# Performance work log

Measured on AMD Instinct MI355X. Metric: run time of the kernel, lower is better.

The kernel has to match this reference:

```python
import jax, jax.numpy as jnp
import numpy as np
from jax import lax

# Model dims (match init_kwargs): hidden=1024, H=8 heads, Dk=Dv=64, N=4 experts, top-1 read/write
H, DK, DV, N_EXP, CHUNK = 8, 64, 64, 4, 64
LORA, GATE_LR = 64, 16          # lora inner dim = head_v_dim, gate low-rank dim
NORMALIZER = 16.0               # gate_logit_normalizer
EPS = 1e-5


def chunk_gla(q, k, v, gk, C=CHUNK):
    """Chunked gated linear attention.
    q,k,gk: [L,H,Dk]; v: [L,H,Dv]; gk is per-dim log decay (<=0).
    Recurrence: S_t = diag(exp(gk_t)) S_{t-1} + k_t^T v_t ; o_t = q_t S_t.
    """
    L, h, dk = q.shape
    dv = v.shape[-1]
    nc = L // C
    qc, kc, vc, gc = (t.reshape(nc, C, h, -1) for t in (q, k, v, gk))
    g = jnp.cumsum(gc, axis=1)            # inclusive within-chunk cumsum [nc,C,h,dk]
    g_last = g[:, -1]                     # [nc,h,dk]
    qg = qc * jnp.exp(g)
    kg = kc * jnp.exp(-g)
    # intra-chunk causal part: A[t,s] = sum_d q_t,d k_s,d exp(g_t,d - g_s,d), s<=t
    A = jnp.einsum('cthd,cshd->chts', qg, kg)
    A = A * jnp.tril(jnp.ones((C, C), q.dtype))
    o_intra = jnp.einsum('chts,cshe->cthe', A, vc)
    # inter-chunk recurrence over chunk-level states
    k_out = kc * jnp.exp(g_last[:, None] - g)          # decay to chunk end
    chunk_kv = jnp.einsum('cthd,cthe->chde', k_out, vc)  # [nc,h,dk,dv]
    decay = jnp.exp(g_last)                            # [nc,h,dk]

    def step(S, inp):
        kv, dec, qg_c = inp
        o_inter = jnp.einsum('thd,hde->the', qg_c, S)
        return S * dec[..., None] + kv, o_inter

    S0 = jnp.zeros((h, dk, dv), q.dtype)
    _, o_inter = lax.scan(step, S0, (chunk_kv, decay, qg))
    return (o_intra + o_inter).reshape(L, h, dv)


def setup_inputs() -> dict:
    key = jax.random.key(0)
    ks = jax.random.split(key, 20)
    B, L, Dh = 1, 4096, 1024
    KD, VD = H * DK, H * DV
    w = lambda i, shape: jax.random.normal(ks[i], shape, jnp.float32) * 0.02
    return {
        'x': jax.random.normal(ks[0], (B, L, Dh), jnp.float32),
        'Wq': w(1, (Dh, KD)), 'Wk': w(2, (Dh, KD)), 'Wv': w(3, (Dh, VD)),
        'Wqa': w(4, (Dh, LORA)), 'Wqb': w(5, (LORA, KD)),
        'Wka': w(6, (Dh, LORA)), 'Wkb': w(7, (LORA, KD)),
        'Wg1a': w(8, (Dh, GATE_LR)), 'Wg1b': w(9, (GATE_LR, KD)), 'bg1': jnp.zeros((KD,), jnp.float32),
        'Wg2a': w(10, (Dh, GATE_LR)), 'Wg2b': w(11, (GATE_LR, KD)), 'bg2': jnp.zeros((KD,), jnp.float32),
        'We': w(12, (Dh, N_EXP)),
        'Wga': w(13, (Dh, LORA)), 'Wgb': w(14, (LORA, VD)),
        'norm_w': jnp.ones((DV,), jnp.float32),
        'Wo': w(15, (VD, Dh)),
    }


def reference(x, Wq, Wk, Wv, Wqa, Wqb, Wka, Wkb, Wg1a, Wg1b, bg1, Wg2a, Wg2b, bg2, We, Wga, Wgb, norm_w, Wo):
    B, L, Dh = x.shape
    scale = DK ** -0.5
    q1 = (x @ Wq).reshape(B, L, H, DK) * scale
    k1 = (x @ Wk).reshape(B, L, H, DK)
    v = (x @ Wv).reshape(B, L, H, DV)
    # low-rank SSE projections; use_k_softmax=True -> softmax over head dim for sparse keys
    q2 = ((x @ Wqa) @ Wqb).reshape(B, L, H, DK) * scale
    k2 = jax.nn.softmax(((x @ Wka) @ Wkb).reshape(B, L, H, DK), axis=-1)
    gk1 = (jax.nn.log_sigmoid((x @ Wg1a) @ Wg1b + bg1) / NORMALIZER).reshape(B, L, H, DK)
    gk2 = (jax.nn.log_sigmoid((x @ Wg2a) @ Wg2b + bg2) / NORMALIZER).reshape(B, L, H, DK)
    # expert routing: softmax + top-1 (num_writer=num_reader=1)
    e = jax.nn.softmax(x @ We, axis=-1)                       # [B,L,N]
    _, idx = lax.top_k(e, 1)
    mask = jax.nn.one_hot(idx, N_EXP, dtype=x.dtype).sum(-2)  # [B,L,N] write/read mask
    rw = e * mask                                             # routing prob at selected experts (emulq/emulk)
    fac = jnp.swapaxes(rw, 1, 2)[:, :, :, None, None]         # [B,N,L,1,1]
    mfac = jnp.swapaxes(mask, 1, 2)[:, :, :, None, None]
    # per-expert routed streams: tokens not routed to expert n neither write (k,gk masked) nor read (q masked)
    q_e = q2[:, None] * fac     # emulq: read gate scales q
    k_e = k2[:, None] * fac     # emulk: write gate scales k
    gk_e = gk2[:, None] * mfac  # state of expert n only decays when written
    gla_b = jax.vmap(chunk_gla)
    o_dense = gla_b(q1, k1, v, gk1)
    gla_be = jax.vmap(jax.vmap(chunk_gla, in_axes=(0, 0, None, 0)))
    o_sparse = gla_be(q_e, k_e, v, gk_e).sum(axis=1)          # sum over experts -> [B,L,H,DV]
    o = o_dense + o_sparse
    # gated RMSNorm + output projection
    g = ((x @ Wga) @ Wgb).reshape(B, L, H, DV)
    o = o * lax.rsqrt(jnp.mean(o * o, axis=-1, keepdims=True) + EPS) * norm_w
    o = o * (g * jax.nn.sigmoid(g))
    return o.reshape(B, L, H * DV) @ Wo
```

## Files before the change

### kernel.cpp

```cpp
#include <hip/hip_runtime.h>
#include <math.h>

#define LL   4096
#define HH   8
#define DK_  64
#define DV_  64
#define KD_  512
#define NEXP 4

typedef __attribute__((ext_vector_type(8))) short  s16x8;
typedef __attribute__((ext_vector_type(4))) float  f32x4;

__device__ __forceinline__ unsigned short f2bf(float f) {
    unsigned u = __float_as_uint(f);
    u += 0x7FFFu + ((u >> 16) & 1u);
    return (unsigned short)(u >> 16);
}

__device__ __forceinline__ void split2(float v, unsigned short& h, unsigned short& l) {
    h = f2bf(v);
    float hf = __uint_as_float((unsigned)h << 16);
    l = f2bf(v - hf);
}

__global__ void cvt_splitA(const float* __restrict__ in, unsigned short* __restrict__ out,
                           int n, int kshift)
{
    int i = blockIdx.x * 256 + threadIdx.x;
    if (i >= n) return;
    unsigned short h, l;
    split2(in[i], h, l);
    int K = 1 << kshift;
    int m = i >> kshift, k = i & (K - 1);
    size_t ro = (size_t)m * 3 * K;
    out[ro + k]         = h;
    out[ro + K + k]     = l;
    out[ro + 2 * K + k] = h;
}

__global__ void cvt_weights_all(
    const float* __restrict__ Wq,  const float* __restrict__ Wk,  const float* __restrict__ Wv,
    const float* __restrict__ Wqa, const float* __restrict__ Wka, const float* __restrict__ Wga,
    const float* __restrict__ Wg1a,const float* __restrict__ Wg2a,const float* __restrict__ We,
    const float* __restrict__ Wo,  const float* __restrict__ Wqb, const float* __restrict__ Wkb,
    const float* __restrict__ Wgb, const float* __restrict__ Wg1b,const float* __restrict__ Wg2b,
    unsigned short* __restrict__ WallT2, unsigned short* __restrict__ WoT2,
    unsigned short* __restrict__ WqbT2,  unsigned short* __restrict__ WkbT2,
    unsigned short* __restrict__ WgbT2,  unsigned short* __restrict__ Wg1bT2,
    unsigned short* __restrict__ Wg2bT2)
{
    int z = blockIdx.z;
    const float* W; unsigned short* WT; int K, N, ldr, pad = 0;
    switch (z) {
        case 0:  W = Wq;   WT = WallT2;                       K = 1024; N = 512;  ldr = 3072; break;
        case 1:  W = Wk;   WT = WallT2 + (size_t)512 * 3072;  K = 1024; N = 512;  ldr = 3072; break;
        case 2:  W = Wv;   WT = WallT2 + (size_t)1024 * 3072; K = 1024; N = 512;  ldr = 3072; break;
        case 3:  W = Wqa;  WT = WallT2 + (size_t)1536 * 3072; K = 1024; N = 64;   ldr = 3072; break;
        case 4:  W = Wka;  WT = WallT2 + (size_t)1600 * 3072; K = 1024; N = 64;   ldr = 3072; break;
        case 5:  W = Wga;  WT = WallT2 + (size_t)1664 * 3072; K = 1024; N = 64;   ldr = 3072; break;
        case 6:  W = Wg1a; WT = WallT2 + (size_t)1728 * 3072; K = 1024; N = 16;   ldr = 3072; break;
        case 7:  W = Wg2a; WT = WallT2 + (size_t)1744 * 3072; K = 1024; N = 16;   ldr = 3072; break;
        case 8:  W = We;   WT = WallT2 + (size_t)1760 * 3072; K = 1024; N = 4;    ldr = 3072; break;
        case 9:  W = Wo;   WT = WoT2;   K = 512; N = 1024; ldr = 1536; break;
        case 10: W = Wqb;  WT = WqbT2;  K = 64;  N = 512;  ldr = 192;  break;
        case 11: W = Wkb;  WT = WkbT2;  K = 64;  N = 512;  ldr = 192;  break;
        case 12: W = Wgb;  WT = WgbT2;  K = 64;  N = 512;  ldr = 192;  break;
        case 13: W = Wg1b; WT = Wg1bT2; K = 16;  N = 512;  ldr = 64; pad = 1; break;
        default: W = Wg2b; WT = Wg2bT2; K = 16;  N = 512;  ldr = 64; pad = 1; break;
    }
    int bx = blockIdx.x * 32, by = blockIdx.y * 32;
    if (bx >= N || by >= K) return;

    __shared__ float t[32][33];
    int x = threadIdx.x, y = threadIdx.y;
    #pragma unroll
    for (int i = 0; i < 4; ++i) {
        int kk = by + y + 8 * i;
        t[y + 8 * i][x] = (bx + x < N && kk < K) ? W[(size_t)kk * N + bx + x] : 0.f;
    }
    __syncthreads();
    #pragma unroll
    for (int i = 0; i < 4; ++i) {
        int n = bx + y + 8 * i;
        int kidx = by + x;
        if (n < N && kidx < K) {
            unsigned short h, l;
            split2(t[x][y + 8 * i], h, l);
            size_t ro = (size_t)n * ldr + kidx;
            WT[ro]         = h;
            WT[ro + K]     = h;
            WT[ro + 2 * K] = l;
        }
        if (pad && n < N && x < 16)
            WT[(size_t)n * ldr + 3 * K + x] = 0;
    }
}

__global__ __launch_bounds__(256) void gemm_qkvcat(
    const unsigned short* __restrict__ A, const unsigned short* __restrict__ B,
    float* __restrict__ Cq, float* __restrict__ Ck, float* __restrict__ Cv,
    float* __restrict__ Ct, int M, int K)
{
    __shared__ __align__(16) unsigned short sm[2 * 128 * 64];
    unsigned short* As = sm;
    unsigned short* Bs = sm + 128 * 64;

    int bxi = blockIdx.x, byi = blockIdx.y;
    {
        int gx = gridDim.x, nwg = gx * gridDim.y;
        int b = byi * gx + bxi;
        int s = (b & 7) * (nwg >> 3) + (b >> 3);
        bxi = s % gx; byi = s / gx;
    }

    int tid  = threadIdx.x;
    int lane = tid & 63;
    int w    = tid >> 6;
    int m0 = byi * 128, n0 = bxi * 128;
    int wr = w >> 1, wc = w & 1;

    f32x4 acc[4][4];
    #pragma unroll
    for (int i = 0; i < 4; ++i)
        #pragma unroll
        for (int j = 0; j < 4; ++j)
            acc[i][j] = (f32x4){0.f, 0.f, 0.f, 0.f};

    const int srow = (lane >> 3);
    const int scb  = ((lane & 7) * 16) ^ (srow << 4);

    for (int kt = 0; kt < K; kt += 64) {
        __syncthreads();
        #pragma unroll
        for (int q = 0; q < 4; ++q) {
            int r = w * 32 + q * 8 + srow;
            const char* ga = (const char*)A + ((size_t)(m0 + r) * K + kt) * 2 + scb;
            const char* gb = (const char*)B + ((size_t)(n0 + r) * K + kt) * 2 + scb;
            __builtin_amdgcn_global_load_lds(
                (const __attribute__((address_space(1))) void*)ga,
                (__attribute__((address_space(3))) void*)((char*)As + (w * 32 + q * 8) * 128),
                16, 0, 0);
            __builtin_amdgcn_global_load_lds(
                (const __attribute__((address_space(1))) void*)gb,
                (__attribute__((address_space(3))) void*)((char*)Bs + (w * 32 + q * 8) * 128),
                16, 0, 0);
        }
        __syncthreads();

        #pragma unroll
        for (int kk = 0; kk < 2; ++kk) {
            int kb = kk * 64 + (lane >> 4) * 16;
            s16x8 af[4], bfr[4];
            #pragma unroll
            for (int mi = 0; mi < 4; ++mi) {
                int r = wr * 64 + mi * 16 + (lane & 15);
                af[mi] = *(const s16x8*)((const char*)As + r * 128 + (kb ^ ((r & 7) << 4)));
            }
            #pragma unroll
            for (int ni = 0; ni < 4; ++ni) {
                int r = wc * 64 + ni * 16 + (lane & 15);
                bfr[ni] = *(const s16x8*)((const char*)Bs + r * 128 + (kb ^ ((r & 7) << 4)));
            }
            #pragma unroll
            for (int mi = 0; mi < 4; ++mi)
                #pragma unroll
                for (int ni = 0; ni < 4; ++ni)
                    acc[mi][ni] = __builtin_amdgcn_mfma_f32_16x16x32_bf16(
                        af[mi], bfr[ni], acc[mi][ni], 0, 0, 0);
        }
    }

    int base = n0 >> 9;
    float* C;
    int ldc, cb;
    if (base == 0)      { C = Cq; ldc = 512; cb = 0; }
    else if (base == 1) { C = Ck; ldc = 512; cb = 512; }
    else if (base == 2) { C = Cv; ldc = 512; cb = 1024; }
    else                { C = Ct; ldc = 256; cb = 1536; }

    #pragma unroll
    for (int mi = 0; mi < 4; ++mi)
        #pragma unroll
        for (int ni = 0; ni < 4; ++ni) {
            int col = n0 + wc * 64 + ni * 16 + (lane & 15) - cb;
            int rb  = m0 + wr * 64 + mi * 16 + (lane >> 4) * 4;
            #pragma unroll
            for (int j = 0; j < 4; ++j)
                C[(size_t)(rb + j) * ldc + col] = acc[mi][ni][j];
        }
}

__global__ __launch_bounds__(256) void gemm_mfma(
    const unsigned short* __restrict__ A0, const unsigned short* __restrict__ A1,
    const unsigned short* __restrict__ A2,
    const unsigned short* __restrict__ B0, const unsigned short* __restrict__ B1,
    const unsigned short* __restrict__ B2,
    float* __restrict__ C0, float* __restrict__ C1, float* __restrict__ C2,
    int M, int N, int K)
{
    const unsigned short* A = (blockIdx.z == 0) ? A0 : (blockIdx.z == 1) ? A1 : A2;
    const unsigned short* B = (blockIdx.z == 0) ? B0 : (blockIdx.z == 1) ? B1 : B2;
    float*                C = (blockIdx.z == 0) ? C0 : (blockIdx.z == 1) ? C1 : C2;

    __shared__ __align__(16) unsigned short sm[2 * 128 * 64];
    unsigned short* As = sm;
    unsigned short* Bs = sm + 128 * 64;

    int bxi = blockIdx.x, byi = blockIdx.y;
    {
        int gx = gridDim.x, nwg = gx * gridDim.y;
        if ((nwg & 7) == 0) {
            int b = byi * gx + bxi;
            int s = (b & 7) * (nwg >> 3) + (b >> 3);
            bxi = s % gx; byi = s / gx;
        }
    }

    int tid  = threadIdx.x;
    int lane = tid & 63;
    int w    = tid >> 6;
    int m0 = byi * 128, n0 = bxi * 128;
    int wr = w >> 1, wc = w & 1;

    f32x4 acc[4][4];
    #pragma unroll
    for (int i = 0; i < 4; ++i)
        #pragma unroll
        for (int j = 0; j < 4; ++j)
            acc[i][j] = (f32x4){0.f, 0.f, 0.f, 0.f};

    const int srow = (lane >> 3);
    const int scb  = ((lane & 7) * 16) ^ (srow << 4);

    for (int kt = 0; kt < K; kt += 64) {
        __syncthreads();
        #pragma unroll
        for (int q = 0; q < 4; ++q) {
            int r = w * 32 + q * 8 + srow;
            const char* ga = (const char*)A + ((size_t)(m0 + r) * K + kt) * 2 + scb;
            const char* gb = (const char*)B + ((size_t)(n0 + r) * K + kt) * 2 + scb;
            __builtin_amdgcn_global_load_lds(
                (const __attribute__((address_space(1))) void*)ga,
                (__attribute__((address_space(3))) void*)((char*)As + (w * 32 + q * 8) * 128),
                16, 0, 0);
            __builtin_amdgcn_global_load_lds(
                (const __attribute__((address_space(1))) void*)gb,
                (__attribute__((address_space(3))) void*)((char*)Bs + (w * 32 + q * 8) * 128),
                16, 0, 0);
        }
        __syncthreads();

        #pragma unroll
        for (int kk = 0; kk < 2; ++kk) {
            int kb = kk * 64 + (lane >> 4) * 16;
            s16x8 af[4], bfr[4];
            #pragma unroll
            for (int mi = 0; mi < 4; ++mi) {
                int r = wr * 64 + mi * 16 + (lane & 15);
                af[mi] = *(const s16x8*)((const char*)As + r * 128 + (kb ^ ((r & 7) << 4)));
            }
            #pragma unroll
            for (int ni = 0; ni < 4; ++ni) {
                int r = wc * 64 + ni * 16 + (lane & 15);
                bfr[ni] = *(const s16x8*)((const char*)Bs + r * 128 + (kb ^ ((r & 7) << 4)));
            }
            #pragma unroll
            for (int mi = 0; mi < 4; ++mi)
                #pragma unroll
                for (int ni = 0; ni < 4; ++ni)
                    acc[mi][ni] = __builtin_amdgcn_mfma_f32_16x16x32_bf16(
                        af[mi], bfr[ni], acc[mi][ni], 0, 0, 0);
        }
    }

    #pragma unroll
    for (int mi = 0; mi < 4; ++mi)
        #pragma unroll
        for (int ni = 0; ni < 4; ++ni) {
            int col = n0 + wc * 64 + ni * 16 + (lane & 15);
            int rb  = m0 + wr * 64 + mi * 16 + (lane >> 4) * 4;
            #pragma unroll
            for (int j = 0; j < 4; ++j)
                C[(size_t)(rb + j) * N + col] = acc[mi][ni][j];
        }
}

__global__ __launch_bounds__(256) void gemm_mfma5(
    const unsigned short* __restrict__ A0, const unsigned short* __restrict__ A1,
    const unsigned short* __restrict__ A2, const unsigned short* __restrict__ A3,
    const unsigned short* __restrict__ A4,
    const unsigned short* __restrict__ B0, const unsigned short* __restrict__ B1,
    const unsigned short* __restrict__ B2, const unsigned short* __restrict__ B3,
    const unsigned short* __restrict__ B4,
    float* __restrict__ C0, float* __restrict__ C1, float* __restrict__ C2,
    float* __restrict__ C3, float* __restrict__ C4, int M, int N)
{
    int z = blockIdx.z;
    const unsigned short* A = (z == 0) ? A0 : (z == 1) ? A1 : (z == 2) ? A2 : (z == 3) ? A3 : A4;
    const unsigned short* B = (z == 0) ? B0 : (z == 1) ? B1 : (z == 2) ? B2 : (z == 3) ? B3 : B4;
    float*                C = (z == 0) ? C0 : (z == 1) ? C1 : (z == 2) ? C2 : (z == 3) ? C3 : C4;
    int K = (z < 3) ? 192 : 64;

    __shared__ __align__(16) unsigned short sm[2 * 128 * 64];
    unsigned short* As = sm;
    unsigned short* Bs = sm + 128 * 64;

    int bxi = blockIdx.x, byi = blockIdx.y;
    {
        int gx = gridDim.x, nwg = gx * gridDim.y;
        if ((nwg & 7) == 0) {
            int b = byi * gx + bxi;
            int s = (b & 7) * (nwg >> 3) + (b >> 3);
            bxi = s % gx; byi = s / gx;
        }
    }

    int tid  = threadIdx.x;
    int lane = tid & 63;
    int w    = tid >> 6;
    int m0 = byi * 128, n0 = bxi * 128;
    int wr = w >> 1, wc = w & 1;

    f32x4 acc[4][4];
    #pragma unroll
    for (int i = 0; i < 4; ++i)
        #pragma unroll
        for (int j = 0; j < 4; ++j)
            acc[i][j] = (f32x4){0.f, 0.f, 0.f, 0.f};

    const int srow = (lane >> 3);
    const int scb  = ((lane & 7) * 16) ^ (srow << 4);

    for (int kt = 0; kt < K; kt += 64) {
        __syncthreads();
        #pragma unroll
        for (int q = 0; q < 4; ++q) {
            int r = w * 32 + q * 8 + srow;
            const char* ga = (const char*)A + ((size_t)(m0 + r) * K + kt) * 2 + scb;
            const char* gb = (const char*)B + ((size_t)(n0 + r) * K + kt) * 2 + scb;
            __builtin_amdgcn_global_load_lds(
                (const __attribute__((address_space(1))) void*)ga,
                (__attribute__((address_space(3))) void*)((char*)As + (w * 32 + q * 8) * 128),
                16, 0, 0);
            __builtin_amdgcn_global_load_lds(
                (const __attribute__((address_space(1))) void*)gb,
                (__attribute__((address_space(3))) void*)((char*)Bs + (w * 32 + q * 8) * 128),
                16, 0, 0);
        }
        __syncthreads();

        #pragma unroll
        for (int kk = 0; kk < 2; ++kk) {
            int kb = kk * 64 + (lane >> 4) * 16;
            s16x8 af[4], bfr[4];
            #pragma unroll
            for (int mi = 0; mi < 4; ++mi) {
                int r = wr * 64 + mi * 16 + (lane & 15);
                af[mi] = *(const s16x8*)((const char*)As + r * 128 + (kb ^ ((r & 7) << 4)));
            }
            #pragma unroll
            for (int ni = 0; ni < 4; ++ni) {
                int r = wc * 64 + ni * 16 + (lane & 15);
                bfr[ni] = *(const s16x8*)((const char*)Bs + r * 128 + (kb ^ ((r & 7) << 4)));
            }
            #pragma unroll
            for (int mi = 0; mi < 4; ++mi)
                #pragma unroll
                for (int ni = 0; ni < 4; ++ni)
                    acc[mi][ni] = __builtin_amdgcn_mfma_f32_16x16x32_bf16(
                        af[mi], bfr[ni], acc[mi][ni], 0, 0, 0);
        }
    }

    #pragma unroll
    for (int mi = 0; mi < 4; ++mi)
        #pragma unroll
        for (int ni = 0; ni < 4; ++ni) {
            int col = n0 + wc * 64 + ni * 16 + (lane & 15);
            int rb  = m0 + wr * 64 + mi * 16 + (lane >> 4) * 4;
            #pragma unroll
            for (int j = 0; j < 4; ++j)
                C[(size_t)(rb + j) * N + col] = acc[mi][ni][j];
        }
}

__global__ void unpack_cat(const float* __restrict__ tcat,
                           unsigned short* __restrict__ tqab2,
                           unsigned short* __restrict__ tkab2,
                           unsigned short* __restrict__ tgab2,
                           unsigned short* __restrict__ tg1s2,
                           unsigned short* __restrict__ tg2s2,
                           float* __restrict__ elog)
{
    int m = blockIdx.x;
    int c = threadIdx.x;
    float vx = tcat[(size_t)m * 256 + c];
    if (c < 192) {
        unsigned short h, l;
        split2(vx, h, l);
        unsigned short* dst = (c < 64) ? tqab2 : (c < 128) ? tkab2 : tgab2;
        int cc = c & 63;
        size_t ro = (size_t)m * 192;
        dst[ro + cc]       = h;
        dst[ro + 64 + cc]  = l;
        dst[ro + 128 + cc] = h;
    } else if (c < 224) {
        unsigned short h, l;
        split2(vx, h, l);
        unsigned short* dst = (c < 208) ? tg1s2 : tg2s2;
        int cc = (c - 192) & 15;
        size_t ro = (size_t)m * 64;
        dst[ro + cc]      = h;
        dst[ro + 16 + cc] = l;
        dst[ro + 32 + cc] = h;
        dst[ro + 48 + cc] = 0;
    } else if (c < 228) {
        elog[(size_t)m * 4 + (c - 224)] = vx;
    }
}

__device__ inline float logsig(float x) {
    return fminf(x, 0.f) - log1pf(expf(-fabsf(x)));
}

__global__ void elementwise_pre(float* __restrict__ q1, float* __restrict__ q2,
                                float* __restrict__ k2, float* __restrict__ gk1,
                                float* __restrict__ gk2,
                                const float* __restrict__ bg1, const float* __restrict__ bg2,
                                const float* __restrict__ elog, float* __restrict__ rw)
{
    int l = blockIdx.x;
    int tid = threadIdx.x;
    int w = tid >> 6, lane = tid & 63;
    int idx = l * KD_ + (w << 6) + lane;

    q1[idx] *= 0.125f;
    q2[idx] *= 0.125f;

    float kv = k2[idx];
    float m = kv;
    for (int s = 32; s >= 1; s >>= 1) m = fmaxf(m, __shfl_xor(m, s, 64));
    float ev = expf(kv - m);
    float ssum = ev;
    for (int s = 32; s >= 1; s >>= 1) ssum += __shfl_xor(ssum, s, 64);
    k2[idx] = ev / ssum;

    int bi = (w << 6) + lane;
    gk1[idx] = logsig(gk1[idx] + bg1[bi]) * (1.f / 16.f);
    gk2[idx] = logsig(gk2[idx] + bg2[bi]) * (1.f / 16.f);

    if (tid == 0) {
        float xs[4];
        float mm = -1e30f;
        for (int j = 0; j < 4; ++j) { xs[j] = elog[l * 4 + j]; mm = fmaxf(mm, xs[j]); }
        float s4 = 0.f;
        for (int j = 0; j < 4; ++j) { xs[j] = expf(xs[j] - mm); s4 += xs[j]; }
        for (int j = 0; j < 4; ++j) xs[j] /= s4;
        int arg = 0; float best = xs[0];
        for (int j = 1; j < 4; ++j) if (xs[j] > best) { best = xs[j]; arg = j; }
        for (int j = 0; j < 4; ++j) rw[l * 4 + j] = (j == arg) ? xs[j] : 0.f;
    }
}

__global__ void gla_kv(const float* __restrict__ k1, const float* __restrict__ k2,
                       const float* __restrict__ gk1, const float* __restrict__ gk2,
                       const float* __restrict__ v, const float* __restrict__ rw,
                       float* __restrict__ kv_all, float* __restrict__ decay_all)
{
    int flat = (blockIdx.z * 8 + blockIdx.y) * 5 + blockIdx.x;
    int sfl = (flat & 7) * 320 + (flat >> 3);
    int p = sfl % 5, h = (sfl / 5) & 7, c = sfl / 40;

    const float* kp = (p == 0) ? k1 : k2;
    const float* gp = (p == 0) ? gk1 : gk2;

    __shared__ __align__(16) unsigned short kgT[64][200];
    __shared__ __align__(16) unsigned short vT[64][200];
    __shared__ float glast[64];
    __shared__ float wrow[64];
    __shared__ float segsum[4][64];

    int tid = threadIdx.x;
    int lane = tid & 63, w = tid >> 6;
    int d = lane, seg = w;

    float gkv[16], kvv[16], vv_[16];
    #pragma unroll
    for (int i = 0; i < 16; ++i) {
        size_t base = (size_t)(c * 64 + seg * 16 + i) * KD_ + (h << 6) + d;
        gkv[i] = gp[base];
        kvv[i] = kp[base];
        vv_[i] = v[base];
    }
    if (tid < 64) {
        int lg = c * 64 + tid;
        wrow[tid] = (p == 0) ? 1.f : rw[lg * 4 + (p - 1)];
    }
    __syncthreads();

    {
        float s = 0.f;
        #pragma unroll
        for (int i = 0; i < 16; ++i) {
            int t = seg * 16 + i;
            float xg = gkv[i];
            if (p > 0 && !(wrow[t] > 0.f)) xg = 0.f;
            s += xg;
            gkv[i] = s;
        }
        segsum[seg][d] = s;
    }
    __syncthreads();
    {
        float off = 0.f, tot = 0.f;
        #pragma unroll
        for (int ss = 0; ss < 4; ++ss) {
            float x = segsum[ss][d];
            tot += x;
            if (ss < seg) off += x;
        }
        if (seg == 0) glast[d] = tot;
        #pragma unroll
        for (int i = 0; i < 16; ++i) {
            int t = seg * 16 + i;
            float g = off + gkv[i];
            float kgval = kvv[i] * wrow[t] * expf(-g);
            unsigned short hh, ll;
            split2(kgval, hh, ll);
            kgT[d][t] = hh; kgT[d][64 + t] = ll; kgT[d][128 + t] = hh;
            split2(vv_[i], hh, ll);
            vT[d][t] = hh; vT[d][64 + t] = hh; vT[d][128 + t] = ll;
        }
    }
    __syncthreads();

    size_t base = (size_t)((c * 8 + h) * 5 + p) * 4096;
    int ar = 16 * w + (lane & 15);
    int kb = (lane >> 4) * 16;
    float dec_[4];
    #pragma unroll
    for (int j = 0; j < 4; ++j) dec_[j] = expf(glast[16 * w + (lane >> 4) * 4 + j]);

    #pragma unroll
    for (int ni = 0; ni < 4; ++ni) {
        f32x4 acc = (f32x4){0.f, 0.f, 0.f, 0.f};
        int br = 16 * ni + (lane & 15);
        #pragma unroll
        for (int kk = 0; kk < 6; ++kk) {
            s16x8 af = *(const s16x8*)((const char*)&kgT[ar][0] + kk * 64 + kb);
            s16x8 bf = *(const s16x8*)((const char*)&vT[br][0] + kk * 64 + kb);
            acc = __builtin_amdgcn_mfma_f32_16x16x32_bf16(af, bf, acc, 0, 0, 0);
        }
        #pragma unroll
        for (int j = 0; j < 4; ++j) {
            int dd = 16 * w + (lane >> 4) * 4 + j;
            kv_all[base + dd * 64 + 16 * ni + (lane & 15)] = acc[j] * dec_[j];
        }
    }
    if (tid < 64) decay_all[(size_t)((c * 8 + h) * 5 + p) * 64 + tid] = expf(glast[tid]);
}

__global__ void gla_state_scan(float* __restrict__ kv, const float* __restrict__ decay)
{
    int gid = blockIdx.x * 256 + threadIdx.x;
    int sub = gid >> 6;
    const size_t stride = 8 * 5 * 64 * 64;
    float S = 0.f;
    float kvv = kv[gid];
    for (int c = 0; c < 64; ++c) {
        size_t o = (size_t)c * stride + gid;
        float nxt = (c < 63) ? kv[o + stride] : 0.f;
        float dec = decay[c * 2560 + sub];
        kv[o] = S;
        S = fmaf(dec, S, kvv);
        kvv = nxt;
    }
}

__global__ void gla_o(const float* __restrict__ q1, const float* __restrict__ q2,
                      const float* __restrict__ k1, const float* __restrict__ k2,
                      const float* __restrict__ gk1, const float* __restrict__ gk2,
                      const float* __restrict__ v, const float* __restrict__ rw,
                      const float* __restrict__ Spre,
                      float* __restrict__ o_dense, float* __restrict__ o_sparse)
{
    int flat = (blockIdx.z * 8 + blockIdx.y) * 5 + blockIdx.x;
    int sfl = (flat & 7) * 320 + (flat >> 3);
    int p = sfl % 5, h = (sfl / 5) & 7, c = sfl / 40;

    const float* qp = (p == 0) ? q1 : q2;
    const float* kp = (p == 0) ? k1 : k2;
    const float* gp = (p == 0) ? gk1 : gk2;

    __shared__ __align__(16) unsigned short qg_bf[64][72];
    __shared__ __align__(16) unsigned short kg_bf[64][72];
    __shared__ __align__(16) unsigned short A_bf[64][72];
    __shared__ __align__(16) unsigned short vT_bf[64][72];
    __shared__ __align__(16) unsigned short ST_bf[64][72];
    __shared__ float wrow[64];
    __shared__ float segsum[4][64];

    int tid = threadIdx.x;
    int lane = tid & 63, w = tid >> 6;
    int d = lane, seg = w;

    {
        float gkv[16], qv[16], kvv[16];
        #pragma unroll
        for (int i = 0; i < 16; ++i) {
            size_t base = (size_t)(c * 64 + seg * 16 + i) * KD_ + (h << 6) + d;
            gkv[i] = gp[base];
            qv[i]  = qp[base];
            kvv[i] = kp[base];
        }
        if (tid < 64) {
            int lg = c * 64 + tid;
            wrow[tid] = (p == 0) ? 1.f : rw[lg * 4 + (p - 1)];
        }
        __syncthreads();

        float s = 0.f;
        #pragma unroll
        for (int i = 0; i < 16; ++i) {
            int t = seg * 16 + i;
            float xg = gkv[i];
            if (p > 0 && !(wrow[t] > 0.f)) xg = 0.f;
            s += xg;
            gkv[i] = s;
        }
        segsum[seg][d] = s;
        __syncthreads();

        float off = 0.f;
        for (int ss = 0; ss < seg; ++ss) off += segsum[ss][d];
        #pragma unroll
        for (int i = 0; i < 16; ++i) {
            int t = seg * 16 + i;
            float g = off + gkv[i];
            float wv = wrow[t];
            qg_bf[t][d] = f2bf(qv[i] * wv * expf(g));
            kg_bf[t][d] = f2bf(kvv[i] * wv * expf(-g));
        }
    }

    {
        size_t sbase = (size_t)((c * 8 + h) * 5 + p) * 4096;
        float Sv[16], vv_[16];
        #pragma unroll
        for (int i = 0; i < 16; ++i) Sv[i] = Spre[sbase + tid + (i << 8)];
        #pragma unroll
        for (int i = 0; i < 16; ++i)
            vv_[i] = v[(size_t)(c * 64 + seg * 16 + i) * KD_ + (h << 6) + d];
        #pragma unroll
        for (int i = 0; i < 16; ++i) ST_bf[d][4 * i + seg] = f2bf(Sv[i]);
        #pragma unroll
        for (int i = 0; i < 16; ++i) vT_bf[d][seg * 16 + i] = f2bf(vv_[i]);
    }
    __syncthreads();

    int am = 16 * w + (lane & 15);
    int kb = (lane >> 4) * 16;

    #pragma unroll
    for (int ni = 0; ni < 4; ++ni) {
        f32x4 acc = (f32x4){0.f, 0.f, 0.f, 0.f};
        if (ni <= w) {
            int br = 16 * ni + (lane & 15);
            #pragma unroll
            for (int kk = 0; kk < 2; ++kk) {
                s16x8 af = *(const s16x8*)((const char*)&qg_bf[am][0] + kk * 64 + kb);
                s16x8 bf = *(const s16x8*)((const char*)&kg_bf[br][0] + kk * 64 + kb);
                acc = __builtin_amdgcn_mfma_f32_16x16x32_bf16(af, bf, acc, 0, 0, 0);
            }
        }
        #pragma unroll
        for (int j = 0; j < 4; ++j) {
            int t = 16 * w + (lane >> 4) * 4 + j;
            int s = 16 * ni + (lane & 15);
            A_bf[t][s] = (s <= t) ? f2bf(acc[j]) : (unsigned short)0;
        }
    }
    __syncthreads();

    #pragma unroll
    for (int ni = 0; ni < 4; ++ni) {
        f32x4 acc = (f32x4){0.f, 0.f, 0.f, 0.f};
        int br = 16 * ni + (lane & 15);
        #pragma unroll
        for (int kk = 0; kk < 2; ++kk) {
            s16x8 af = *(const s16x8*)((const char*)&qg_bf[am][0] + kk * 64 + kb);
            s16x8 bf = *(const s16x8*)((const char*)&ST_bf[br][0] + kk * 64 + kb);
            acc = __builtin_amdgcn_mfma_f32_16x16x32_bf16(af, bf, acc, 0, 0, 0);
        }
        #pragma unroll
        for (int kk = 0; kk < 2; ++kk) {
            s16x8 af = *(const s16x8*)((const char*)&A_bf[am][0] + kk * 64 + kb);
            s16x8 bf = *(const s16x8*)((const char*)&vT_bf[br][0] + kk * 64 + kb);
            acc = __builtin_amdgcn_mfma_f32_16x16x32_bf16(af, bf, acc, 0, 0, 0);
        }
        #pragma unroll
        for (int j = 0; j < 4; ++j) {
            int t = 16 * w + (lane >> 4) * 4 + j;
            int e = 16 * ni + (lane & 15);
            size_t idx = (size_t)(c * 64 + t) * KD_ + (h << 6) + e;
            if (p == 0)                 o_dense[idx]  = acc[j];
            else if (wrow[t] > 0.f)     o_sparse[idx] = acc[j];
        }
    }
}

__global__ void postnorm(const float* __restrict__ o_dense, const float* __restrict__ o_sparse,
                         const float* __restrict__ gbuf,
                         const float* __restrict__ norm_w, unsigned short* __restrict__ og2)
{
    int l = blockIdx.x;
    int tid = threadIdx.x;
    int w = tid >> 6, lane = tid & 63;
    int bi = (w << 6) + lane;
    int idx = l * KD_ + bi;
    float o = o_dense[idx] + o_sparse[idx];
    float ss = o * o;
    for (int s = 32; s >= 1; s >>= 1) ss += __shfl_xor(ss, s, 64);
    float r = rsqrtf(ss * (1.f / 64.f) + 1e-5f);
    float val = o * r * norm_w[lane];
    float gv = gbuf[idx];
    val *= gv / (1.f + expf(-gv));
    unsigned short h, lo;
    split2(val, h, lo);
    size_t ro = (size_t)l * (3 * KD_) + bi;
    og2[ro]           = h;
    og2[ro + KD_]     = lo;
    og2[ro + 2 * KD_] = h;
}

extern "C" void kernel_launch(void* const* d_in, const int* in_sizes, int n_in,
                              void* d_out, int out_size, void* d_ws, size_t ws_size,
                              hipStream_t stream)
{
    const float* x    = (const float*)d_in[0];
    const float* Wq   = (const float*)d_in[1];
    const float* Wk   = (const float*)d_in[2];
    const float* Wv   = (const float*)d_in[3];
    const float* Wqa  = (const float*)d_in[4];
    const float* Wqb  = (const float*)d_in[5];
    const float* Wka  = (const float*)d_in[6];
    const float* Wkb  = (const float*)d_in[7];
    const float* Wg1a = (const float*)d_in[8];
    const float* Wg1b = (const float*)d_in[9];
    const float* bg1  = (const float*)d_in[10];
    const float* Wg2a = (const float*)d_in[11];
    const float* Wg2b = (const float*)d_in[12];
    const float* bg2  = (const float*)d_in[13];
    const float* We   = (const float*)d_in[14];
    const float* Wga  = (const float*)d_in[15];
    const float* Wgb  = (const float*)d_in[16];
    const float* normw= (const float*)d_in[17];
    const float* Wo   = (const float*)d_in[18];

    float* ws = (float*)d_ws;
    const size_t LKD = (size_t)LL * KD_;
    float* q1   = ws;
    float* k1   = q1 + LKD;
    float* v    = k1 + LKD;
    float* q2   = v  + LKD;
    float* k2   = q2 + LKD;
    float* gk1  = k2 + LKD;
    float* gk2  = gk1 + LKD;
    float* o_dense  = gk2 + LKD;
    float* o_sparse = o_dense + LKD;
    float* gbuf = o_sparse + LKD;
    float* elog = gbuf + LKD;
    float* rw   = elog + (size_t)LL * 4;
    float* kv_all    = rw + (size_t)LL * 4;
    float* decay_all = kv_all + (size_t)64 * 8 * 5 * 64 * 64;

    unsigned short* bp = (unsigned short*)(decay_all + 163840);
    unsigned short* WallT2 = bp; bp += (size_t)1792 * 3072;
    unsigned short* WoT2   = bp; bp += (size_t)1024 * 1536;
    unsigned short* WqbT2  = bp; bp += (size_t)512 * 192;
    unsigned short* WkbT2  = bp; bp += (size_t)512 * 192;
    unsigned short* WgbT2  = bp; bp += (size_t)512 * 192;
    unsigned short* Wg1bT2 = bp; bp += (size_t)512 * 64;
    unsigned short* Wg2bT2 = bp; bp += (size_t)512 * 64;
    unsigned short* tqab2  = bp; bp += (size_t)LL * 192;
    unsigned short* tkab2  = bp; bp += (size_t)LL * 192;
    unsigned short* tgab2  = bp; bp += (size_t)LL * 192;
    unsigned short* tg1s2  = bp; bp += (size_t)LL * 64;
    unsigned short* tg2s2  = bp; bp += (size_t)LL * 64;
    float* tcat = (float*)bp;

    unsigned short* xb2 = (unsigned short*)kv_all;
    unsigned short* og2 = (unsigned short*)kv_all;

    dim3 blk(256);
    dim3 tblk(32, 8);

    cvt_splitA<<<dim3((LL * 1024 + 255) / 256), blk, 0, stream>>>(x, xb2, LL * 1024, 10);
    hipMemsetAsync(WallT2 + (size_t)1764 * 3072, 0, (size_t)(1792 - 1764) * 3072 * 2, stream);
    cvt_weights_all<<<dim3(32, 32, 15), tblk, 0, stream>>>(
        Wq, Wk, Wv, Wqa, Wka, Wga, Wg1a, Wg2a, We, Wo, Wqb, Wkb, Wgb, Wg1b, Wg2b,
        WallT2, WoT2, WqbT2, WkbT2, WgbT2, Wg1bT2, Wg2bT2);

    gemm_qkvcat<<<dim3(14, 32), blk, 0, stream>>>(xb2, WallT2, q1, k1, v, tcat, LL, 3072);
    unpack_cat<<<dim3(LL), blk, 0, stream>>>(tcat, tqab2, tkab2, tgab2, tg1s2, tg2s2, elog);

    gemm_mfma5<<<dim3(4, 32, 5), blk, 0, stream>>>(
        tqab2, tkab2, tgab2, tg1s2, tg2s2,
        WqbT2, WkbT2, WgbT2, Wg1bT2, Wg2bT2,
        q2, k2, gbuf, gk1, gk2, LL, KD_);

    elementwise_pre<<<LL, 512, 0, stream>>>(q1, q2, k2, gk1, gk2, bg1, bg2, elog, rw);

    gla_kv<<<dim3(5, 8, 64), blk, 0, stream>>>(k1, k2, gk1, gk2, v, rw, kv_all, decay_all);
    gla_state_scan<<<dim3(640), blk, 0, stream>>>(kv_all, decay_all);
    gla_o<<<dim3(5, 8, 64), blk, 0, stream>>>(q1, q2, k1, k2, gk1, gk2, v, rw,
                                              kv_all, o_dense, o_sparse);

    postnorm<<<LL, 512, 0, stream>>>(o_dense, o_sparse, gbuf, normw, og2);

    gemm_mfma<<<dim3(8, 32, 1), blk, 0, stream>>>(og2, og2, og2, WoT2, WoT2, WoT2,
                                                  (float*)d_out, (float*)d_out, (float*)d_out,
                                                  LL, 1024, 1536);
}
```

Measured before the change: 231.7 us.

## Double-buffer GEMM LDS tiles and fuse elementwise prep into GEMM epilogues

All three MFMA GEMM kernels now use two LDS buffers, prefetching the next K tile with global_load_lds while MFMAs run on the current one, so each iteration needs one barrier instead of two. The q scaling, the gate bias add with logsigmoid and the normalizer are moved into the GEMM epilogues. The leftover elementwise kernel becomes a smaller softmax and router kernel, which saves a read-modify-write pass over q1, q2, gk1 and gk2. In exchange, LDS per block doubles to 64KB, which may lower occupancy.

```diff
diff --git a/kernel.cpp b/kernel.cpp
--- a/kernel.cpp
+++ b/kernel.cpp
@@ -21,6 +21,10 @@
     h = f2bf(v);
     float hf = __uint_as_float((unsigned)h << 16);
     l = f2bf(v - hf);
+}
+
+__device__ __forceinline__ float logsig(float x) {
+    return fminf(x, 0.f) - log1pf(expf(-fabsf(x)));
 }
 
 __global__ void cvt_splitA(const float* __restrict__ in, unsigned short* __restrict__ out,
@@ -101,9 +105,7 @@
     float* __restrict__ Cq, float* __restrict__ Ck, float* __restrict__ Cv,
     float* __restrict__ Ct, int M, int K)
 {
-    __shared__ __align__(16) unsigned short sm[2 * 128 * 64];
-    unsigned short* As = sm;
-    unsigned short* Bs = sm + 128 * 64;
+    __shared__ __align__(16) unsigned short sm[4 * 128 * 64];
 
     int bxi = blockIdx.x, byi = blockIdx.y;
     {
@@ -129,8 +131,9 @@
     const int srow = (lane >> 3);
     const int scb  = ((lane & 7) * 16) ^ (srow << 4);
 
-    for (int kt = 0; kt < K; kt += 64) {
-        __syncthreads();
+    auto stage = [&](int buf, int kt) {
+        unsigned short* Asb = sm + buf * (2 * 128 * 64);
+        unsigned short* Bsb = Asb + 128 * 64;
         #pragma unroll
         for (int q = 0; q < 4; ++q) {
             int r = w * 32 + q * 8 + srow;
@@ -138,15 +141,22 @@
             const char* gb = (const char*)B + ((size_t)(n0 + r) * K + kt) * 2 + scb;
             __builtin_amdgcn_global_load_lds(
                 (const __attribute__((address_space(1))) void*)ga,
-                (__attribute__((address_space(3))) void*)((char*)As + (w * 32 + q * 8) * 128),
+                (__attribute__((address_space(3))) void*)((char*)Asb + (w * 32 + q * 8) * 128),
                 16, 0, 0);
             __builtin_amdgcn_global_load_lds(
                 (const __attribute__((address_space(1))) void*)gb,
-                (__attribute__((address_space(3))) void*)((char*)Bs + (w * 32 + q * 8) * 128),
+                (__attribute__((address_space(3))) void*)((char*)Bsb + (w * 32 + q * 8) * 128),
                 16, 0, 0);
         }
-        __syncthreads();
-
+    };
+
+    stage(0, 0);
+    __syncthreads();
+    int cur = 0;
+    for (int kt = 0; kt < K; kt += 64) {
+        if (kt + 64 < K) stage(cur ^ 1, kt + 64);
+        unsigned short* Asb = sm + cur * (2 * 128 * 64);
+        unsigned short* Bsb = Asb + 128 * 64;
         #pragma unroll
         for (int kk = 0; kk < 2; ++kk) {
             int kb = kk * 64 + (lane >> 4) * 16;
@@ -154,12 +164,12 @@
             #pragma unroll
             for (int mi = 0; mi < 4; ++mi) {
                 int r = wr * 64 + mi * 16 + (lane & 15);
-                af[mi] = *(const s16x8*)((const char*)As + r * 128 + (kb ^ ((r & 7) << 4)));
+                af[mi] = *(const s16x8*)((const char*)Asb + r * 128 + (kb ^ ((r & 7) << 4)));
             }
             #pragma unroll
             for (int ni = 0; ni < 4; ++ni) {
                 int r = wc * 64 + ni * 16 + (lane & 15);
-                bfr[ni] = *(const s16x8*)((const char*)Bs + r * 128 + (kb ^ ((r & 7) << 4)));
+                bfr[ni] = *(const s16x8*)((const char*)Bsb + r * 128 + (kb ^ ((r & 7) << 4)));
             }
             #pragma unroll
             for (int mi = 0; mi < 4; ++mi)
@@ -168,12 +178,15 @@
                     acc[mi][ni] = __builtin_amdgcn_mfma_f32_16x16x32_bf16(
                         af[mi], bfr[ni], acc[mi][ni], 0, 0, 0);
         }
+        __syncthreads();
+        cur ^= 1;
     }
 
     int base = n0 >> 9;
     float* C;
     int ldc, cb;
-    if (base == 0)      { C = Cq; ldc = 512; cb = 0; }
+    float scale = 1.f;
+    if (base == 0)      { C = Cq; ldc = 512; cb = 0; scale = 0.125f; }
     else if (base == 1) { C = Ck; ldc = 512; cb = 512; }
     else if (base == 2) { C = Cv; ldc = 512; cb = 1024; }
     else                { C = Ct; ldc = 256; cb = 1536; }
@@ -186,25 +199,15 @@
             int rb  = m0 + wr * 64 + mi * 16 + (lane >> 4) * 4;
             #pragma unroll
             for (int j = 0; j < 4; ++j)
-                C[(size_t)(rb + j) * ldc + col] = acc[mi][ni][j];
+                C[(size_t)(rb + j) * ldc + col] = acc[mi][ni][j] * scale;
         }
 }
 
 __global__ __launch_bounds__(256) void gemm_mfma(
-    const unsigned short* __restrict__ A0, const unsigned short* __restrict__ A1,
-    const unsigned short* __restrict__ A2,
-    const unsigned short* __restrict__ B0, const unsigned short* __restrict__ B1,
-    const unsigned short* __restrict__ B2,
-    float* __restrict__ C0, float* __restrict__ C1, float* __restrict__ C2,
-    int M, int N, int K)
-{
-    const unsigned short* A = (blockIdx.z == 0) ? A0 : (blockIdx.z == 1) ? A1 : A2;
-    const unsigned short* B = (blockIdx.z == 0) ? B0 : (blockIdx.z == 1) ? B1 : B2;
-    float*                C = (blockIdx.z == 0) ? C0 : (blockIdx.z == 1) ? C1 : C2;
-
-    __shared__ __align__(16) unsigned short sm[2 * 128 * 64];
-    unsigned short* As = sm;
-    unsigned short* Bs = sm + 128 * 64;
+    const unsigned short* __restrict__ A, const unsigned short* __restrict__ B,
+    float* __restrict__ C, int M, int N, int K)
+{
+    __shared__ __align__(16) unsigned short sm[4 * 128 * 64];
 
     int bxi = blockIdx.x, byi = blockIdx.y;
     {
@@ -232,8 +235,9 @@
     const int srow = (lane >> 3);
     const int scb  = ((lane & 7) * 16) ^ (srow << 4);
 
-    for (int kt = 0; kt < K; kt += 64) {
-        __syncthreads();
+    auto stage = [&](int buf, int kt) {
+        unsigned short* Asb = sm + buf * (2 * 128 * 64);
+        unsigned short* Bsb = Asb + 128 * 64;
         #pragma unroll
         for (int q = 0; q < 4; ++q) {
             int r = w * 32 + q * 8 + srow;
@@ -241,15 +245,22 @@
             const char* gb = (const char*)B + ((size_t)(n0 + r) * K + kt) * 2 + scb;
             __builtin_amdgcn_global_load_lds(
                 (const __attribute__((address_space(1))) void*)ga,
-                (__attribute__((address_space(3))) void*)((char*)As + (w * 32 + q * 8) * 128),
+                (__attribute__((address_space(3))) void*)((char*)Asb + (w * 32 + q * 8) * 128),
                 16, 0, 0);
             __builtin_amdgcn_global_load_lds(
                 (const __attribute__((address_space(1))) void*)gb,
-                (__attribute__((address_space(3))) void*)((char*)Bs + (w * 32 + q * 8) * 128),
+                (__attribute__((address_space(3))) void*)((char*)Bsb + (w * 32 + q * 8) * 128),
                 16, 0, 0);
         }
-        __syncthreads();
-
+    };
+
+    stage(0, 0);
+    __syncthreads();
+    int cur = 0;
+    for (int kt = 0; kt < K; kt += 64) {
+        if (kt + 64 < K) stage(cur ^ 1, kt + 64);
+        unsigned short* Asb = sm + cur * (2 * 128 * 64);
+        unsigned short* Bsb = Asb + 128 * 64;
         #pragma unroll
         for (int kk = 0; kk < 2; ++kk) {
             int kb = kk * 64 + (lane >> 4) * 16;
@@ -257,12 +268,12 @@
             #pragma unroll
             for (int mi = 0; mi < 4; ++mi) {
                 int r = wr * 64 + mi * 16 + (lane & 15);
-                af[mi] = *(const s16x8*)((const char*)As + r * 128 + (kb ^ ((r & 7) << 4)));
+                af[mi] = *(const s16x8*)((const char*)Asb + r * 128 + (kb ^ ((r & 7) << 4)));
             }
             #pragma unroll
             for (int ni = 0; ni < 4; ++ni) {
                 int r = wc * 64 + ni * 16 + (lane & 15);
-                bfr[ni] = *(const s16x8*)((const char*)Bs + r * 128 + (kb ^ ((r & 7) << 4)));
+                bfr[ni] = *(const s16x8*)((const char*)Bsb + r * 128 + (kb ^ ((r & 7) << 4)));
             }
             #pragma unroll
             for (int mi = 0; mi < 4; ++mi)
@@ -271,6 +282,8 @@
                     acc[mi][ni] = __builtin_amdgcn_mfma_f32_16x16x32_bf16(
                         af[mi], bfr[ni], acc[mi][ni], 0, 0, 0);
         }
+        __syncthreads();
+        cur ^= 1;
     }
 
     #pragma unroll
@@ -293,17 +306,17 @@
     const unsigned short* __restrict__ B2, const unsigned short* __restrict__ B3,
     const unsigned short* __restrict__ B4,
     float* __restrict__ C0, float* __restrict__ C1, float* __restrict__ C2,
-    float* __restrict__ C3, float* __restrict__ C4, int M, int N)
+    float* __restrict__ C3, float* __restrict__ C4,
+    const float* __restrict__ bg1, const float* __restrict__ bg2, int M, int N)
 {
     int z = blockIdx.z;
     const unsigned short* A = (z == 0) ? A0 : (z == 1) ? A1 : (z == 2) ? A2 : (z == 3) ? A3 : A4;
     const unsigned short* B = (z == 0) ? B0 : (z == 1) ? B1 : (z == 2) ? B2 : (z == 3) ? B3 : B4;
     float*                C = (z == 0) ? C0 : (z == 1) ? C1 : (z == 2) ? C2 : (z == 3) ? C3 : C4;
     int K = (z < 3) ? 192 : 64;
-
-    __shared__ __align__(16) unsigned short sm[2 * 128 * 64];
-    unsigned short* As = sm;
-    unsigned short* Bs = sm + 128 * 64;
+    const float* bg = (z == 3) ? bg1 : bg2;
+
+    __shared__ __align__(16) unsigned short sm[4 * 128 * 64];
 
     int bxi = blockIdx.x, byi = blockIdx.y;
     {
@@ -331,8 +344,9 @@
     const int srow = (lane >> 3);
     const int scb  = ((lane & 7) * 16) ^ (srow << 4);
 
-    for (int kt = 0; kt < K; kt += 64) {
-        __syncthreads();
+    auto stage = [&](int buf, int kt) {
+        unsigned short* Asb = sm + buf * (2 * 128 * 64);
+        unsigned short* Bsb = Asb + 128 * 64;
         #pragma unroll
         for (int q = 0; q < 4; ++q) {
             int r = w * 32 + q * 8 + srow;
@@ -340,15 +354,22 @@
             const char* gb = (const char*)B + ((size_t)(n0 + r) * K + kt) * 2 + scb;
             __builtin_amdgcn_global_load_lds(
                 (const __attribute__((address_space(1))) void*)ga,
-                (__attribute__((address_space(3))) void*)((char*)As + (w * 32 + q * 8) * 128),
+                (__attribute__((address_space(3))) void*)((char*)Asb + (w * 32 + q * 8) * 128),
                 16, 0, 0);
             __builtin_amdgcn_global_load_lds(
                 (const __attribute__((address_space(1))) void*)gb,
-                (__attribute__((address_space(3))) void*)((char*)Bs + (w * 32 + q * 8) * 128),
+                (__attribute__((address_space(3))) void*)((char*)Bsb + (w * 32 + q * 8) * 128),
                 16, 0, 0);
         }
-        __syncthreads();
-
+    };
+
+    stage(0, 0);
+    __syncthreads();
+    int cur = 0;
+    for (int kt = 0; kt < K; kt += 64) {
+        if (kt + 64 < K) stage(cur ^ 1, kt + 64);
+        unsigned short* Asb = sm + cur * (2 * 128 * 64);
+        unsigned short* Bsb = Asb + 128 * 64;
         #pragma unroll
         for (int kk = 0; kk < 2; ++kk) {
             int kb = kk * 64 + (lane >> 4) * 16;
@@ -356,12 +377,12 @@
             #pragma unroll
             for (int mi = 0; mi < 4; ++mi) {
                 int r = wr * 64 + mi * 16 + (lane & 15);
-                af[mi] = *(const s16x8*)((const char*)As + r * 128 + (kb ^ ((r & 7) << 4)));
+                af[mi] = *(const s16x8*)((const char*)Asb + r * 128 + (kb ^ ((r & 7) << 4)));
             }
             #pragma unroll
             for (int ni = 0; ni < 4; ++ni) {
                 int r = wc * 64 + ni * 16 + (lane & 15);
-                bfr[ni] = *(const s16x8*)((const char*)Bs + r * 128 + (kb ^ ((r & 7) << 4)));
+                bfr[ni] = *(const s16x8*)((const char*)Bsb + r * 128 + (kb ^ ((r & 7) << 4)));
             }
             #pragma unroll
             for (int mi = 0; mi < 4; ++mi)
@@ -370,6 +391,8 @@
                     acc[mi][ni] = __builtin_amdgcn_mfma_f32_16x16x32_bf16(
                         af[mi], bfr[ni], acc[mi][ni], 0, 0, 0);
         }
+        __syncthreads();
+        cur ^= 1;
     }
 
     #pragma unroll
@@ -379,8 +402,12 @@
             int col = n0 + wc * 64 + ni * 16 + (lane & 15);
             int rb  = m0 + wr * 64 + mi * 16 + (lane >> 4) * 4;
             #pragma unroll
-            for (int j = 0; j < 4; ++j)
-                C[(size_t)(rb + j) * N + col] = acc[mi][ni][j];
+            for (int j = 0; j < 4; ++j) {
+                float vvv = acc[mi][ni][j];
+                if (z == 0)      vvv *= 0.125f;
+                else if (z >= 3) vvv = logsig(vvv + bg[col]) * 0.0625f;
+                C[(size_t)(rb + j) * N + col] = vvv;
+            }
         }
 }
 
@@ -419,23 +446,13 @@
     }
 }
 
-__device__ inline float logsig(float x) {
-    return fminf(x, 0.f) - log1pf(expf(-fabsf(x)));
-}
-
-__global__ void elementwise_pre(float* __restrict__ q1, float* __restrict__ q2,
-                                float* __restrict__ k2, float* __restrict__ gk1,
-                                float* __restrict__ gk2,
-                                const float* __restrict__ bg1, const float* __restrict__ bg2,
-                                const float* __restrict__ elog, float* __restrict__ rw)
+__global__ void softmax_router(float* __restrict__ k2, const float* __restrict__ elog,
+                               float* __restrict__ rw)
 {
     int l = blockIdx.x;
     int tid = threadIdx.x;
     int w = tid >> 6, lane = tid & 63;
     int idx = l * KD_ + (w << 6) + lane;
-
-    q1[idx] *= 0.125f;
-    q2[idx] *= 0.125f;
 
     float kv = k2[idx];
     float m = kv;
@@ -444,10 +461,6 @@
     float ssum = ev;
     for (int s = 32; s >= 1; s >>= 1) ssum += __shfl_xor(ssum, s, 64);
     k2[idx] = ev / ssum;
-
-    int bi = (w << 6) + lane;
-    gk1[idx] = logsig(gk1[idx] + bg1[bi]) * (1.f / 16.f);
-    gk2[idx] = logsig(gk2[idx] + bg2[bi]) * (1.f / 16.f);
 
     if (tid == 0) {
         float xs[4];
@@ -807,9 +820,9 @@
     gemm_mfma5<<<dim3(4, 32, 5), blk, 0, stream>>>(
         tqab2, tkab2, tgab2, tg1s2, tg2s2,
         WqbT2, WkbT2, WgbT2, Wg1bT2, Wg2bT2,
-        q2, k2, gbuf, gk1, gk2, LL, KD_);
-
-    elementwise_pre<<<LL, 512, 0, stream>>>(q1, q2, k2, gk1, gk2, bg1, bg2, elog, rw);
+        q2, k2, gbuf, gk1, gk2, bg1, bg2, LL, KD_);
+
+    softmax_router<<<LL, 512, 0, stream>>>(k2, elog, rw);
 
     gla_kv<<<dim3(5, 8, 64), blk, 0, stream>>>(k1, k2, gk1, gk2, v, rw, kv_all, decay_all);
     gla_state_scan<<<dim3(640), blk, 0, stream>>>(kv_all, decay_all);
@@ -818,7 +831,5 @@
 
     postnorm<<<LL, 512, 0, stream>>>(o_dense, o_sparse, gbuf, normw, og2);
 
-    gemm_mfma<<<dim3(8, 32, 1), blk, 0, stream>>>(og2, og2, og2, WoT2, WoT2, WoT2,
-                                                  (float*)d_out, (float*)d_out, (float*)d_out,
-                                                  LL, 1024, 1536);
-}
+    gemm_mfma<<<dim3(8, 32), blk, 0, stream>>>(og2, WoT2, (float*)d_out, LL, 1024, 1536);
+}
```

New measurement: 312.8 us (median of 2 runs). 1.35x slower.
